# Performance work log

Measured on AMD Instinct MI355X. Metric: run time of the kernel, lower is better.

## Reference

```python
import jax, jax.numpy as jnp
import numpy as np
from jax import lax

B, IMG, ED, NC = 32, 224, 256, 10
DI, DS, DC, DR = 512, 64, 4, 16   # d_inner, d_state, d_conv, dt_rank
NB, L = 6, (IMG // 16) ** 2       # 6 mamba blocks, seq len 196
EPS = 1e-5


def setup_inputs():
    key = jax.random.key(0)
    ks = iter(jax.random.split(key, 48))
    def rn(shape, s=0.02):
        return jax.random.normal(next(ks), shape, jnp.float32) * s
    def ru(shape):
        return jax.random.uniform(next(ks), shape, jnp.float32, 0.5, 1.5)
    inp = {"x": jax.random.normal(next(ks), (B, 3, IMG, IMG), jnp.float32)}
    c = [ED // 4, ED // 2, ED]
    for i, (ci, co) in enumerate([(3, c[0]), (c[0], c[1]), (c[1], c[2])], 1):
        inp[f"c{i}w"] = rn((co, ci, 3, 3), 0.05)
        inp[f"c{i}b"] = rn((co,))
        inp[f"b{i}g"] = jnp.ones((co,), jnp.float32)
        inp[f"b{i}b"] = jnp.zeros((co,), jnp.float32)
        inp[f"b{i}m"] = rn((co,))
        inp[f"b{i}v"] = ru((co,))
    inp["ln_g"] = jnp.ones((NB, ED), jnp.float32)
    inp["ln_b"] = jnp.zeros((NB, ED), jnp.float32)
    inp["w_in"] = rn((NB, 2 * DI, ED))
    inp["cw"] = rn((NB, DI, DC), 0.1)
    inp["cb"] = rn((NB, DI))
    inp["w_x"] = rn((NB, DR + 2 * DS, DI))
    inp["w_dt"] = rn((NB, DI, DR), 0.1)
    inp["b_dt"] = rn((NB, DI), 0.5)
    inp["a_log"] = jnp.tile(jnp.log(jnp.arange(1, DS + 1, dtype=jnp.float32)), (NB, DI, 1))
    inp["d_skip"] = jnp.ones((NB, DI), jnp.float32)
    inp["w_out"] = rn((NB, ED, DI))
    inp["fc_w"] = rn((NC, ED))
    inp["fc_b"] = jnp.zeros((NC,), jnp.float32)
    return inp


def _conv2d(x, w, s, p):
    return lax.conv_general_dilated(x, w, (s, s), [(p, p), (p, p)],
                                    dimension_numbers=("NCHW", "OIHW", "NCHW"))


def _bn(x, g, b, m, v):
    sh = (1, -1, 1, 1)
    return (x - m.reshape(sh)) * (g.reshape(sh) / jnp.sqrt(v.reshape(sh) + EPS)) + b.reshape(sh)


def _maxpool(x, k, s, p):
    return lax.reduce_window(x, -jnp.inf, lax.max, (1, 1, k, k), (1, 1, s, s),
                             [(0, 0), (0, 0), (p, p), (p, p)])


def _mamba_block(x, ln_g, ln_b, w_in, cw, cb, w_x, w_dt, b_dt, a_log, d_skip, w_out):
    res = x
    mu = x.mean(-1, keepdims=True)
    var = ((x - mu) ** 2).mean(-1, keepdims=True)
    h = (x - mu) / jnp.sqrt(var + EPS) * ln_g + ln_b
    xz = jnp.einsum("bld,ed->ble", h, w_in)            # [B,L,2*DI]
    xi, z = xz[..., :DI], xz[..., DI:]
    # causal depthwise conv1d (pad left DC-1) + silu
    xt = lax.conv_general_dilated(xi.transpose(0, 2, 1), cw[:, None, :], (1,),
                                  [(DC - 1, 0)], dimension_numbers=("NCH", "OIH", "NCH"),
                                  feature_group_count=DI) + cb[None, :, None]
    xc = jax.nn.silu(xt).transpose(0, 2, 1)            # [B,L,DI]
    dbl = jnp.einsum("bld,ed->ble", xc, w_x)           # [B,L,DR+2*DS]
    dt = jax.nn.softplus(jnp.einsum("blr,dr->bld", dbl[..., :DR], w_dt) + b_dt)
    Bm = dbl[..., DR:DR + DS]                          # [B,L,DS]
    Cm = dbl[..., DR + DS:]                            # [B,L,DS]
    A = -jnp.exp(a_log)                                # [DI,DS]

    def step(hst, ins):
        dt_t, b_t, c_t, x_t = ins                      # [B,DI],[B,DS],[B,DS],[B,DI]
        dA = jnp.exp(dt_t[..., None] * A)              # [B,DI,DS]
        hst = dA * hst + (dt_t * x_t)[..., None] * b_t[:, None, :]
        return hst, jnp.einsum("bds,bs->bd", hst, c_t)

    h0 = jnp.zeros((x.shape[0], DI, DS), x.dtype)
    _, ys = lax.scan(step, h0, (dt.transpose(1, 0, 2), Bm.transpose(1, 0, 2),
                                Cm.transpose(1, 0, 2), xc.transpose(1, 0, 2)))
    y = ys.transpose(1, 0, 2) + d_skip * xc
    y = y * jax.nn.silu(z)
    return jnp.einsum("bld,ed->ble", y, w_out) + res


def reference(x, c1w, c1b, b1g, b1b, b1m, b1v, c2w, c2b, b2g, b2b, b2m, b2v,
              c3w, c3b, b3g, b3b, b3m, b3v, ln_g, ln_b, w_in, cw, cb, w_x,
              w_dt, b_dt, a_log, d_skip, w_out, fc_w, fc_b):
    h = _maxpool(jax.nn.relu(_bn(_conv2d(x, c1w, 2, 1) + c1b.reshape(1, -1, 1, 1), b1g, b1b, b1m, b1v)), 3, 2, 1)
    h = _maxpool(jax.nn.relu(_bn(_conv2d(h, c2w, 1, 1) + c2b.reshape(1, -1, 1, 1), b2g, b2b, b2m, b2v)), 2, 2, 0)
    h = _maxpool(jax.nn.relu(_bn(_conv2d(h, c3w, 1, 1) + c3b.reshape(1, -1, 1, 1), b3g, b3b, b3m, b3v)), 2, 2, 0)
    h = h.reshape(h.shape[0], ED, -1).transpose(0, 2, 1)   # [B,L,ED]
    for i in range(NB):
        h = _mamba_block(h, ln_g[i], ln_b[i], w_in[i], cw[i], cb[i], w_x[i],
                         w_dt[i], b_dt[i], a_log[i], d_skip[i], w_out[i])
    h = h.mean(axis=1)                                     # adaptive avg pool over L
    return h @ fc_w.T + fc_b
```

## Files before the change

kernel.cpp:

```cpp
#include <hip/hip_runtime.h>

typedef __bf16 bf16x8 __attribute__((ext_vector_type(8)));
typedef float f32x4 __attribute__((ext_vector_type(4)));

#define EPS 1e-5f

__device__ __forceinline__ unsigned short f2bu(float f) {
  union { float f; unsigned u; } x; x.f = f;
  unsigned r = x.u + 0x7fffu + ((x.u >> 16) & 1u);
  return (unsigned short)(r >> 16);
}
__device__ __forceinline__ float bu2f(unsigned short u) {
  union { unsigned u; float f; } x; x.u = ((unsigned)u) << 16;
  return x.f;
}

__device__ __forceinline__ void gld16(const void* g, void* l) {
  __builtin_amdgcn_global_load_lds((const __attribute__((address_space(1))) void*)g,
                                   (__attribute__((address_space(3))) void*)l, 16, 0, 0);
}

__global__ __launch_bounds__(256) void k_f2b(const float* __restrict__ in,
                                             unsigned short* __restrict__ out, int n) {
  int i = blockIdx.x * 256 + threadIdx.x;
  if (i < n) out[i] = f2bu(in[i]);
}

template <int CI>
__global__ __launch_bounds__(256) void k_repack(const float* __restrict__ w,
                                                unsigned short* __restrict__ out, int n) {
  int id = blockIdx.x * 256 + threadIdx.x;
  if (id >= n) return;
  int ci = id % CI;
  int tap = (id / CI) % 9;
  int co = id / (9 * CI);
  out[id] = f2bu(w[(co * CI + ci) * 9 + tap]);
}

__global__ __launch_bounds__(256) void k_wdt_t(const float* __restrict__ in,
                                               float* __restrict__ out) {
  int id = blockIdx.x * 256 + threadIdx.x;
  int d = id & 511;
  int r = (id >> 9) & 15;
  int blk = id >> 13;
  out[id] = in[(blk * 512 + d) * 16 + r];
}

__global__ __launch_bounds__(256) void k_conv1a(
    const float* __restrict__ x, const float* __restrict__ w,
    const float* __restrict__ cb, const float* __restrict__ g,
    const float* __restrict__ bb, const float* __restrict__ bm_,
    const float* __restrict__ bv, unsigned short* __restrict__ out) {
  __shared__ float sw[64 * 27];
  __shared__ float sa[64], sb[64];
  for (int i = threadIdx.x; i < 64 * 27; i += 256) sw[i] = w[i];
  if (threadIdx.x < 64) {
    int c = threadIdx.x;
    float alpha = g[c] * rsqrtf(bv[c] + EPS);
    sa[c] = alpha;
    sb[c] = (cb[c] - bm_[c]) * alpha + bb[c];
  }
  __syncthreads();
  int id = blockIdx.x * 256 + threadIdx.x;
  int c = id & 63;
  int t = id >> 6;
  int ox = t % 112; t /= 112;
  int oy = t % 112;
  int b = t / 112;
  const float* xb = x + (size_t)b * 3 * 224 * 224;
  const float* wc = sw + c * 27;
  float acc = 0.f;
#pragma unroll
  for (int ci = 0; ci < 3; ++ci)
#pragma unroll
    for (int ky = 0; ky < 3; ++ky) {
      int iy = oy * 2 - 1 + ky;
      bool vy = (unsigned)iy < 224u;
#pragma unroll
      for (int kx = 0; kx < 3; ++kx) {
        int ix = ox * 2 - 1 + kx;
        float v = (vy && (unsigned)ix < 224u) ? xb[(ci * 224 + iy) * 224 + ix] : 0.f;
        acc = fmaf(v, wc[ci * 9 + ky * 3 + kx], acc);
      }
    }
  out[id] = f2bu(fmaxf(acc * sa[c] + sb[c], 0.f));
}

__global__ __launch_bounds__(256) void k_pool3(const unsigned short* __restrict__ in,
                                               unsigned short* __restrict__ out) {
  int id = blockIdx.x * 256 + threadIdx.x;
  int c = id & 63;
  int t = id >> 6;
  int px = t % 56; t /= 56;
  int py = t % 56;
  int b = t / 56;
  float m = 0.f;
#pragma unroll
  for (int ky = 0; ky < 3; ++ky) {
    int iy = py * 2 - 1 + ky;
    if ((unsigned)iy >= 112u) continue;
#pragma unroll
    for (int kx = 0; kx < 3; ++kx) {
      int ix = px * 2 - 1 + kx;
      if ((unsigned)ix >= 112u) continue;
      m = fmaxf(m, bu2f(in[(((size_t)(b * 112 + iy) * 112) + ix) * 64 + c]));
    }
  }
  out[id] = f2bu(m);
}

template <int H, int Wd, int CI, int CO>
__global__ __launch_bounds__(256) void k_convgemm(
    const unsigned short* __restrict__ In, const unsigned short* __restrict__ Wt,
    const float* __restrict__ cb, const float* __restrict__ g,
    const float* __restrict__ bb, const float* __restrict__ bm_,
    const float* __restrict__ bv, unsigned short* __restrict__ Out) {
  constexpr int K = 9 * CI;
  constexpr int NTN = CO / 64;
  int bm = blockIdx.x / NTN, bn = blockIdx.x - bm * NTN;
  int lane = threadIdx.x & 63, wid = threadIdx.x >> 6;
  int wr = wid >> 1, wc = wid & 1;
  int r0 = bm * 64 + wr * 32 + (lane & 15);
  int r1 = r0 + 16;
  int c0 = bn * 64 + wc * 32 + (lane & 15);
  int koff = (lane >> 4) << 3;
  int ox0 = r0 % Wd; int t0 = r0 / Wd; int oy0 = t0 % H; int b0 = t0 / H;
  int ox1 = r1 % Wd; int t1 = r1 / Wd; int oy1 = t1 % H; int b1 = t1 / H;
  const unsigned short* pb0 = Wt + (size_t)c0 * K + koff;
  const unsigned short* pb1 = Wt + (size_t)(c0 + 16) * K + koff;
  f32x4 acc[2][2] = {};
  for (int k0 = 0; k0 < K; k0 += 32) {
    int k = k0 + koff;
    int tap = k / CI;
    int ci = k - tap * CI;
    int ky = tap / 3, kx = tap - ky * 3;
    int iy0 = oy0 + ky - 1, ix0 = ox0 + kx - 1;
    int iy1 = oy1 + ky - 1, ix1 = ox1 + kx - 1;
    bf16x8 a0 = {};
    bf16x8 a1 = {};
    if ((unsigned)iy0 < (unsigned)H && (unsigned)ix0 < (unsigned)Wd)
      a0 = *(const bf16x8*)(In + ((size_t)((b0 * H + iy0) * Wd + ix0)) * CI + ci);
    if ((unsigned)iy1 < (unsigned)H && (unsigned)ix1 < (unsigned)Wd)
      a1 = *(const bf16x8*)(In + ((size_t)((b1 * H + iy1) * Wd + ix1)) * CI + ci);
    bf16x8 w0 = *(const bf16x8*)(pb0 + k0);
    bf16x8 w1 = *(const bf16x8*)(pb1 + k0);
    acc[0][0] = __builtin_amdgcn_mfma_f32_16x16x32_bf16(a0, w0, acc[0][0], 0, 0, 0);
    acc[0][1] = __builtin_amdgcn_mfma_f32_16x16x32_bf16(a0, w1, acc[0][1], 0, 0, 0);
    acc[1][0] = __builtin_amdgcn_mfma_f32_16x16x32_bf16(a1, w0, acc[1][0], 0, 0, 0);
    acc[1][1] = __builtin_amdgcn_mfma_f32_16x16x32_bf16(a1, w1, acc[1][1], 0, 0, 0);
  }
  int rr = (lane >> 4) * 4, rc = lane & 15;
#pragma unroll
  for (int tj = 0; tj < 2; ++tj) {
    int col = bn * 64 + wc * 32 + tj * 16 + rc;
    float alpha = g[col] * rsqrtf(bv[col] + EPS);
    float beta = (cb[col] - bm_[col]) * alpha + bb[col];
#pragma unroll
    for (int ti = 0; ti < 2; ++ti) {
      int row = bm * 64 + wr * 32 + ti * 16 + rr;
#pragma unroll
      for (int r = 0; r < 4; ++r) {
        float v = fmaxf(acc[ti][tj][r] * alpha + beta, 0.f);
        Out[(size_t)(row + r) * CO + col] = f2bu(v);
      }
    }
  }
}

template <int H, int Wd, int C, bool OUTF>
__global__ __launch_bounds__(256) void k_pool(const unsigned short* __restrict__ in,
                                              void* __restrict__ outv) {
  constexpr int OH = H / 2, OW = Wd / 2;
  int id = blockIdx.x * 256 + threadIdx.x;
  int c = id % C;
  int t = id / C;
  int px = t % OW; t /= OW;
  int py = t % OH;
  int b = t / OH;
  const unsigned short* p = in + (((size_t)(b * H + py * 2) * Wd) + px * 2) * C + c;
  float m0 = bu2f(p[0]), m1 = bu2f(p[C]);
  float m2 = bu2f(p[(size_t)Wd * C]), m3 = bu2f(p[(size_t)Wd * C + C]);
  float m = fmaxf(fmaxf(m0, m1), fmaxf(m2, m3));
  if (OUTF) ((float*)outv)[id] = m;
  else ((unsigned short*)outv)[id] = f2bu(m);
}

__global__ __launch_bounds__(256) void k_ln(const float* __restrict__ h,
                                            const float* __restrict__ g,
                                            const float* __restrict__ b2,
                                            unsigned short* __restrict__ out) {
  int lane = threadIdx.x & 63, wid = threadIdx.x >> 6;
  int t = blockIdx.x * 4 + wid;
  float4 v = *(const float4*)(h + (size_t)t * 256 + lane * 4);
  float s = v.x + v.y + v.z + v.w;
  float q = v.x * v.x + v.y * v.y + v.z * v.z + v.w * v.w;
#pragma unroll
  for (int off = 32; off; off >>= 1) {
    s += __shfl_xor(s, off);
    q += __shfl_xor(q, off);
  }
  float mu = s * (1.f / 256.f);
  float var = q * (1.f / 256.f) - mu * mu;
  float rs = rsqrtf(var + EPS);
  float4 gg = *(const float4*)(g + lane * 4);
  float4 bb = *(const float4*)(b2 + lane * 4);
  ushort4 o;
  o.x = f2bu((v.x - mu) * rs * gg.x + bb.x);
  o.y = f2bu((v.y - mu) * rs * gg.y + bb.y);
  o.z = f2bu((v.z - mu) * rs * gg.z + bb.z);
  o.w = f2bu((v.w - mu) * rs * gg.w + bb.w);
  *(ushort4*)(out + (size_t)t * 256 + lane * 4) = o;
}

template <int BM, int BN, int KSTEPS, bool ADD>
__global__ __launch_bounds__(256) void k_sgemm(const unsigned short* __restrict__ A,
                                               const unsigned short* __restrict__ W,
                                               float* __restrict__ C,
                                               int N, int ntn) {
  constexpr int K = KSTEPS * 64;
  constexpr int MR = BM / 32;
  constexpr int NR = BN / 32;
  __shared__ __align__(16) unsigned short As[BM * 64];
  __shared__ __align__(16) unsigned short Bs[BN * 64];
  int bm = blockIdx.x / ntn, bn = blockIdx.x - bm * ntn;
  int lane = threadIdx.x & 63, wid = threadIdx.x >> 6;
  int wr = wid >> 1, wc = wid & 1;
  const int arow = lane >> 3, acol = (lane & 7) * 8;
  f32x4 acc[MR][NR] = {};
  const unsigned short* Abase = A + (size_t)(bm * BM) * K;
  const unsigned short* Wbase = W + (size_t)(bn * BN) * K;
  for (int t = 0; t < KSTEPS; ++t) {
    int k0 = t * 64;
#pragma unroll
    for (int i = 0; i < BM / 32; ++i) {
      int chunk = wid * (BM / 32) + i;
      gld16(Abase + (size_t)(chunk * 8 + arow) * K + k0 + acol, &As[chunk * 512 + lane * 8]);
    }
#pragma unroll
    for (int i = 0; i < BN / 32; ++i) {
      int chunk = wid * (BN / 32) + i;
      gld16(Wbase + (size_t)(chunk * 8 + arow) * K + k0 + acol, &Bs[chunk * 512 + lane * 8]);
    }
    __syncthreads();
#pragma unroll
    for (int kk = 0; kk < 2; ++kk) {
      bf16x8 af[MR], bfr[NR];
#pragma unroll
      for (int mi = 0; mi < MR; ++mi)
        af[mi] = *(const bf16x8*)&As[(wr * (BM / 2) + mi * 16 + (lane & 15)) * 64 + kk * 32 + (lane >> 4) * 8];
#pragma unroll
      for (int nj = 0; nj < NR; ++nj)
        bfr[nj] = *(const bf16x8*)&Bs[(wc * (BN / 2) + nj * 16 + (lane & 15)) * 64 + kk * 32 + (lane >> 4) * 8];
#pragma unroll
      for (int mi = 0; mi < MR; ++mi)
#pragma unroll
        for (int nj = 0; nj < NR; ++nj)
          acc[mi][nj] = __builtin_amdgcn_mfma_f32_16x16x32_bf16(af[mi], bfr[nj], acc[mi][nj], 0, 0, 0);
    }
    __syncthreads();
  }
  int rr = (lane >> 4) * 4, rc = lane & 15;
#pragma unroll
  for (int mi = 0; mi < MR; ++mi)
#pragma unroll
    for (int nj = 0; nj < NR; ++nj) {
      int row = bm * BM + wr * (BM / 2) + mi * 16 + rr;
      int col = bn * BN + wc * (BN / 2) + nj * 16 + rc;
#pragma unroll
      for (int r = 0; r < 4; ++r) {
        float v = acc[mi][nj][r];
        if (ADD) v += C[(size_t)(row + r) * N + col];
        C[(size_t)(row + r) * N + col] = v;
      }
    }
}

template <bool ADD_RES>
__global__ __launch_bounds__(256) void k_gemm(const unsigned short* __restrict__ A,
                                              const unsigned short* __restrict__ W,
                                              float* __restrict__ C, int M, int N,
                                              int K, int ntn) {
  int bm = blockIdx.x / ntn, bn = blockIdx.x - bm * ntn;
  int lane = threadIdx.x & 63, wid = threadIdx.x >> 6;
  int wr = wid >> 1, wc = wid & 1;
  int r0 = bm * 64 + wr * 32 + (lane & 15);
  int c0 = bn * 64 + wc * 32 + (lane & 15);
  int koff = (lane >> 4) << 3;
  int cc0 = (c0 < N) ? c0 : (N - 1);
  int cc1 = (c0 + 16 < N) ? (c0 + 16) : (N - 1);
  const unsigned short* pa0 = A + (size_t)r0 * K + koff;
  const unsigned short* pa1 = A + (size_t)(r0 + 16) * K + koff;
  const unsigned short* pb0 = W + (size_t)cc0 * K + koff;
  const unsigned short* pb1 = W + (size_t)cc1 * K + koff;
  f32x4 acc[2][2] = {};
  for (int k0 = 0; k0 < K; k0 += 32) {
    bf16x8 a0 = *(const bf16x8*)(pa0 + k0);
    bf16x8 a1 = *(const bf16x8*)(pa1 + k0);
    bf16x8 b0 = *(const bf16x8*)(pb0 + k0);
    bf16x8 b1 = *(const bf16x8*)(pb1 + k0);
    acc[0][0] = __builtin_amdgcn_mfma_f32_16x16x32_bf16(a0, b0, acc[0][0], 0, 0, 0);
    acc[0][1] = __builtin_amdgcn_mfma_f32_16x16x32_bf16(a0, b1, acc[0][1], 0, 0, 0);
    acc[1][0] = __builtin_amdgcn_mfma_f32_16x16x32_bf16(a1, b0, acc[1][0], 0, 0, 0);
    acc[1][1] = __builtin_amdgcn_mfma_f32_16x16x32_bf16(a1, b1, acc[1][1], 0, 0, 0);
  }
  int rr = (lane >> 4) * 4, rc = lane & 15;
#pragma unroll
  for (int ti = 0; ti < 2; ++ti)
#pragma unroll
    for (int tj = 0; tj < 2; ++tj) {
      int col = bn * 64 + wc * 32 + tj * 16 + rc;
      if (col >= N) continue;
      int row = bm * 64 + wr * 32 + ti * 16 + rr;
#pragma unroll
      for (int r = 0; r < 4; ++r) {
        float v = acc[ti][tj][r];
        if (ADD_RES) v += C[(size_t)(row + r) * N + col];
        C[(size_t)(row + r) * N + col] = v;
      }
    }
}

__global__ __launch_bounds__(256) void k_dwconv(const float* __restrict__ xz,
                                                const float* __restrict__ cw,
                                                const float* __restrict__ cb,
                                                float* __restrict__ xc,
                                                unsigned short* __restrict__ xcb) {
  int id = blockIdx.x * 256 + threadIdx.x;
  int d = id & 511;
  int bl = id >> 9;
  int l = bl % 196;
  int b = bl / 196;
  const float* xi = xz + (size_t)(b * 196) * 1024 + d;
  float4 c4 = *(const float4*)(cw + d * 4);
  float acc = cb[d];
  if (l >= 3) acc = fmaf(xi[(size_t)(l - 3) * 1024], c4.x, acc);
  if (l >= 2) acc = fmaf(xi[(size_t)(l - 2) * 1024], c4.y, acc);
  if (l >= 1) acc = fmaf(xi[(size_t)(l - 1) * 1024], c4.z, acc);
  acc = fmaf(xi[(size_t)l * 1024], c4.w, acc);
  float s = acc / (1.f + __expf(-acc));
  xc[id] = s;
  xcb[id] = f2bu(s);
}

__global__ __launch_bounds__(256) void k_dt(const float* __restrict__ dbl,
                                            const float* __restrict__ wt,
                                            const float* __restrict__ bdt,
                                            float* __restrict__ dt) {
  int id = blockIdx.x * 256 + threadIdx.x;
  int d = id & 511;
  int bl = id >> 9;
  const float4* a = (const float4*)(dbl + (size_t)bl * 144);
  float acc = bdt[d];
#pragma unroll
  for (int i = 0; i < 4; ++i) {
    float4 av = a[i];
    acc = fmaf(av.x, wt[(i * 4 + 0) * 512 + d], acc);
    acc = fmaf(av.y, wt[(i * 4 + 1) * 512 + d], acc);
    acc = fmaf(av.z, wt[(i * 4 + 2) * 512 + d], acc);
    acc = fmaf(av.w, wt[(i * 4 + 3) * 512 + d], acc);
  }
  dt[id] = fmaxf(acc, 0.f) + log1pf(__expf(-fabsf(acc)));
}

__global__ __launch_bounds__(256) void k_scan(
    const float* __restrict__ dtb, const float* __restrict__ xc,
    const float* __restrict__ dbl, const float* __restrict__ xz,
    const float* __restrict__ a_log, const float* __restrict__ d_skip,
    unsigned short* __restrict__ y) {
  __shared__ float lds[4][584];
  int lane = threadIdx.x & 63, wid = threadIdx.x >> 6;
  int wgid = blockIdx.x * 4 + wid;
  int b = wgid >> 9, d = wgid & 511;
  float A = -__expf(a_log[d * 64 + lane]);
  float dsk = d_skip[d];
  const float* dt_p = dtb + (size_t)(b * 196) * 512 + d;
  const float* xc_p = xc + (size_t)(b * 196) * 512 + d;
  const float* z_p = xz + (size_t)(b * 196) * 1024 + 512 + d;
  const float* bc_p = dbl + (size_t)(b * 196) * 144 + 16 + lane;
  unsigned short* y_p = y + (size_t)(b * 196) * 512 + d;
  float* L = lds[wid];
  float h = 0.f;
  int g = lane >> 3, j = lane & 7;
  for (int l0 = 0; l0 < 196; l0 += 8) {
    float p[8];
#pragma unroll
    for (int li = 0; li < 8; ++li) {
      int l = l0 + li;
      bool ok = (l < 196);
      float dtv = ok ? dt_p[(size_t)l * 512] : 0.f;
      float xv = ok ? xc_p[(size_t)l * 512] : 0.f;
      float Bv = ok ? bc_p[(size_t)l * 144] : 0.f;
      float Cv = ok ? bc_p[(size_t)l * 144 + 64] : 0.f;
      float dA = __expf(dtv * A);
      h = fmaf(dA, h, (dtv * xv) * Bv);
      p[li] = h * Cv;
    }
#pragma unroll
    for (int li = 0; li < 8; ++li) L[lane * 9 + li] = p[li];
    __builtin_amdgcn_wave_barrier();
    float s = 0.f;
#pragma unroll
    for (int k = 0; k < 8; ++k) s += L[(j * 8 + k) * 9 + g];
    __builtin_amdgcn_wave_barrier();
    s += __shfl_xor(s, 1);
    s += __shfl_xor(s, 2);
    s += __shfl_xor(s, 4);
    int l = l0 + g;
    if (j == 0 && l < 196) {
      float xv = xc_p[(size_t)l * 512];
      float zv = z_p[(size_t)l * 1024];
      float sig = 1.f / (1.f + __expf(-zv));
      y_p[(size_t)l * 512] = f2bu((s + dsk * xv) * (zv * sig));
    }
  }
}

__global__ __launch_bounds__(256) void k_mean(const float* __restrict__ h,
                                              float* __restrict__ pooled) {
  int b = blockIdx.x, e = threadIdx.x;
  float s = 0.f;
  for (int l = 0; l < 196; ++l) s += h[(size_t)(b * 196 + l) * 256 + e];
  pooled[b * 256 + e] = s * (1.f / 196.f);
}

__global__ __launch_bounds__(320) void k_fc(const float* __restrict__ pooled,
                                            const float* __restrict__ fw,
                                            const float* __restrict__ fb,
                                            float* __restrict__ out) {
  int t = threadIdx.x;
  if (t >= 320) return;
  int b = t / 10, n = t - b * 10;
  float s = fb[n];
  for (int e = 0; e < 256; ++e) s += pooled[b * 256 + e] * fw[n * 256 + e];
  out[t] = s;
}

static inline unsigned cdiv(unsigned a, unsigned b) { return (a + b - 1) / b; }

extern "C" void kernel_launch(void* const* d_in, const int* in_sizes, int n_in,
                              void* d_out, int out_size, void* d_ws, size_t ws_size,
                              hipStream_t stream) {
  const float* x = (const float*)d_in[0];
  const float* c1w = (const float*)d_in[1]; const float* c1b = (const float*)d_in[2];
  const float* b1g = (const float*)d_in[3]; const float* b1b = (const float*)d_in[4];
  const float* b1m = (const float*)d_in[5]; const float* b1v = (const float*)d_in[6];
  const float* c2w = (const float*)d_in[7]; const float* c2b = (const float*)d_in[8];
  const float* b2g = (const float*)d_in[9]; const float* b2b = (const float*)d_in[10];
  const float* b2m = (const float*)d_in[11]; const float* b2v = (const float*)d_in[12];
  const float* c3w = (const float*)d_in[13]; const float* c3b = (const float*)d_in[14];
  const float* b3g = (const float*)d_in[15]; const float* b3b = (const float*)d_in[16];
  const float* b3m = (const float*)d_in[17]; const float* b3v = (const float*)d_in[18];
  const float* ln_g = (const float*)d_in[19]; const float* ln_b = (const float*)d_in[20];
  const float* w_in = (const float*)d_in[21];
  const float* cw = (const float*)d_in[22]; const float* cbv = (const float*)d_in[23];
  const float* w_x = (const float*)d_in[24];
  const float* w_dt = (const float*)d_in[25]; const float* b_dt = (const float*)d_in[26];
  const float* a_log = (const float*)d_in[27]; const float* d_skip = (const float*)d_in[28];
  const float* w_out = (const float*)d_in[29];
  const float* fc_w = (const float*)d_in[30]; const float* fc_b = (const float*)d_in[31];

  char* ws = (char*)d_ws;
  size_t off = 0;
  auto take = [&](size_t bytes) { size_t o = off; off += bytes; return o; };
  size_t S = take(67837952);
  unsigned short* c1o = (unsigned short*)(ws + S + 0);
  unsigned short* t1 = (unsigned short*)(ws + S + 51380224);
  unsigned short* t2 = (unsigned short*)(ws + S + 0);
  unsigned short* t3 = (unsigned short*)(ws + S + 25690112);
  unsigned short* t4 = (unsigned short*)(ws + S + 32112640);
  float* xz = (float*)(ws + S + 0);
  float* xc = (float*)(ws + S + 25690112);
  unsigned short* xcb = (unsigned short*)(ws + S + 38535168);
  float* dbl = (float*)(ws + S + 44957696);
  float* dtb = (float*)(ws + S + 48570368);
  unsigned short* ybf = (unsigned short*)(ws + S + 61415424);
  float* h = (float*)(ws + take(6422528));
  unsigned short* hbf = (unsigned short*)(ws + take(3211264));
  unsigned short* w_in_bf = (unsigned short*)(ws + take(3145728));
  unsigned short* w_x_bf = (unsigned short*)(ws + take(884736));
  unsigned short* w_out_bf = (unsigned short*)(ws + take(1572864));
  unsigned short* w2p = (unsigned short*)(ws + take(147456));
  unsigned short* w3p = (unsigned short*)(ws + take(589824));
  float* wdt_t = (float*)(ws + take(196608));
  float* pooled = (float*)(ws + take(32768));
  (void)ws_size; (void)in_sizes; (void)n_in; (void)out_size;

  k_f2b<<<cdiv(1572864, 256), 256, 0, stream>>>(w_in, w_in_bf, 1572864);
  k_f2b<<<cdiv(442368, 256), 256, 0, stream>>>(w_x, w_x_bf, 442368);
  k_f2b<<<cdiv(786432, 256), 256, 0, stream>>>(w_out, w_out_bf, 786432);
  k_repack<64><<<cdiv(73728, 256), 256, 0, stream>>>(c2w, w2p, 73728);
  k_repack<128><<<cdiv(294912, 256), 256, 0, stream>>>(c3w, w3p, 294912);
  k_wdt_t<<<cdiv(49152, 256), 256, 0, stream>>>(w_dt, wdt_t);

  k_conv1a<<<100352, 256, 0, stream>>>(x, c1w, c1b, b1g, b1b, b1m, b1v, c1o);
  k_pool3<<<25088, 256, 0, stream>>>(c1o, t1);
  k_convgemm<56, 56, 64, 128><<<1568 * 2, 256, 0, stream>>>(t1, w2p, c2b, b2g, b2b, b2m, b2v, t2);
  k_pool<56, 56, 128, false><<<12544, 256, 0, stream>>>(t2, t3);
  k_convgemm<28, 28, 128, 256><<<392 * 4, 256, 0, stream>>>(t3, w3p, c3b, b3g, b3b, b3m, b3v, t4);
  k_pool<28, 28, 256, true><<<6272, 256, 0, stream>>>(t4, h);

  for (int blk = 0; blk < 6; ++blk) {
    k_ln<<<1568, 256, 0, stream>>>(h, ln_g + blk * 256, ln_b + blk * 256, hbf);
    k_sgemm<128, 128, 4, false><<<49 * 8, 256, 0, stream>>>(
        hbf, w_in_bf + (size_t)blk * 1024 * 256, xz, 1024, 8);
    k_dwconv<<<12544, 256, 0, stream>>>(xz, cw + blk * 512 * 4, cbv + blk * 512, xc, xcb);
    k_gemm<false><<<98 * 3, 256, 0, stream>>>(xcb, w_x_bf + (size_t)blk * 144 * 512, dbl,
                                              6272, 144, 512, 3);
    k_dt<<<12544, 256, 0, stream>>>(dbl, wdt_t + blk * 8192, b_dt + blk * 512, dtb);
    k_scan<<<4096, 256, 0, stream>>>(dtb, xc, dbl, xz, a_log + blk * 512 * 64,
                                     d_skip + blk * 512, ybf);
    k_sgemm<64, 64, 8, true><<<98 * 4, 256, 0, stream>>>(
        ybf, w_out_bf + (size_t)blk * 256 * 512, h, 256, 4);
  }

  k_mean<<<32, 256, 0, stream>>>(h, pooled);
  k_fc<<<1, 320, 0, stream>>>(pooled, fc_w, fc_b, (float*)d_out);
}
```

Before: 1.939 ms.

## Merge weight-prep launches, specialize conv1 interior path, parallelize pooling head

Six separate weight conversion and repack kernels are merged into one k_prep launch that dispatches on a flat index. The first conv kernel now copies its weights into registers and takes a branch-free path for interior pixels, keeping the bounds-checked path only for edge pixels. The mean-pool and FC head are split across 128 blocks for partial sums, then finished by a per-batch block that uses wave shuffles, replacing the single-block serial FC. Together these aim to cut launch count and serial tail work, at the cost of a few extra index computations and some duplicated code.

```diff
diff --git a/kernel.cpp b/kernel.cpp
--- a/kernel.cpp
+++ b/kernel.cpp
@@ -20,30 +20,36 @@
                                    (__attribute__((address_space(3))) void*)l, 16, 0, 0);
 }
 
-__global__ __launch_bounds__(256) void k_f2b(const float* __restrict__ in,
-                                             unsigned short* __restrict__ out, int n) {
-  int i = blockIdx.x * 256 + threadIdx.x;
-  if (i < n) out[i] = f2bu(in[i]);
-}
-
-template <int CI>
-__global__ __launch_bounds__(256) void k_repack(const float* __restrict__ w,
-                                                unsigned short* __restrict__ out, int n) {
+__global__ __launch_bounds__(256) void k_prep(
+    const float* __restrict__ w_in, unsigned short* __restrict__ w_in_bf,
+    const float* __restrict__ w_x, unsigned short* __restrict__ w_x_bf,
+    const float* __restrict__ w_out, unsigned short* __restrict__ w_out_bf,
+    const float* __restrict__ c2w, unsigned short* __restrict__ w2p,
+    const float* __restrict__ c3w, unsigned short* __restrict__ w3p,
+    const float* __restrict__ w_dt, float* __restrict__ wdt_t) {
   int id = blockIdx.x * 256 + threadIdx.x;
-  if (id >= n) return;
-  int ci = id % CI;
-  int tap = (id / CI) % 9;
-  int co = id / (9 * CI);
-  out[id] = f2bu(w[(co * CI + ci) * 9 + tap]);
-}
-
-__global__ __launch_bounds__(256) void k_wdt_t(const float* __restrict__ in,
-                                               float* __restrict__ out) {
-  int id = blockIdx.x * 256 + threadIdx.x;
-  int d = id & 511;
-  int r = (id >> 9) & 15;
-  int blk = id >> 13;
-  out[id] = in[(blk * 512 + d) * 16 + r];
+  if (id < 1572864) { w_in_bf[id] = f2bu(w_in[id]); return; }
+  id -= 1572864;
+  if (id < 442368) { w_x_bf[id] = f2bu(w_x[id]); return; }
+  id -= 442368;
+  if (id < 786432) { w_out_bf[id] = f2bu(w_out[id]); return; }
+  id -= 786432;
+  if (id < 73728) {
+    int ci = id % 64, tap = (id / 64) % 9, co = id / 576;
+    w2p[id] = f2bu(c2w[(co * 64 + ci) * 9 + tap]);
+    return;
+  }
+  id -= 73728;
+  if (id < 294912) {
+    int ci = id % 128, tap = (id / 128) % 9, co = id / 1152;
+    w3p[id] = f2bu(c3w[(co * 128 + ci) * 9 + tap]);
+    return;
+  }
+  id -= 294912;
+  {
+    int d = id & 511, r = (id >> 9) & 15, blk = id >> 13;
+    wdt_t[id] = w_dt[(blk * 512 + d) * 16 + r];
+  }
 }
 
 __global__ __launch_bounds__(256) void k_conv1a(
@@ -67,23 +73,37 @@
   int ox = t % 112; t /= 112;
   int oy = t % 112;
   int b = t / 112;
-  const float* xb = x + (size_t)b * 3 * 224 * 224;
-  const float* wc = sw + c * 27;
+  float wr[27];
+#pragma unroll
+  for (int i = 0; i < 27; ++i) wr[i] = sw[c * 27 + i];
+  float alpha = sa[c], beta = sb[c];
+  const float* base = x + (size_t)b * 3 * 224 * 224 + (oy * 2 - 1) * 224 + (ox * 2 - 1);
   float acc = 0.f;
-#pragma unroll
-  for (int ci = 0; ci < 3; ++ci)
-#pragma unroll
-    for (int ky = 0; ky < 3; ++ky) {
-      int iy = oy * 2 - 1 + ky;
-      bool vy = (unsigned)iy < 224u;
-#pragma unroll
-      for (int kx = 0; kx < 3; ++kx) {
-        int ix = ox * 2 - 1 + kx;
-        float v = (vy && (unsigned)ix < 224u) ? xb[(ci * 224 + iy) * 224 + ix] : 0.f;
-        acc = fmaf(v, wc[ci * 9 + ky * 3 + kx], acc);
+  if (oy >= 1 && ox >= 1) {
+#pragma unroll
+    for (int ci = 0; ci < 3; ++ci)
+#pragma unroll
+      for (int ky = 0; ky < 3; ++ky)
+#pragma unroll
+        for (int kx = 0; kx < 3; ++kx)
+          acc = fmaf(base[ci * 224 * 224 + ky * 224 + kx], wr[ci * 9 + ky * 3 + kx], acc);
+  } else {
+#pragma unroll
+    for (int ci = 0; ci < 3; ++ci)
+#pragma unroll
+      for (int ky = 0; ky < 3; ++ky) {
+        int iy = oy * 2 - 1 + ky;
+        bool vy = (unsigned)iy < 224u;
+#pragma unroll
+        for (int kx = 0; kx < 3; ++kx) {
+          int ix = ox * 2 - 1 + kx;
+          float v = (vy && (unsigned)ix < 224u)
+                        ? x[(size_t)b * 3 * 224 * 224 + (ci * 224 + iy) * 224 + ix] : 0.f;
+          acc = fmaf(v, wr[ci * 9 + ky * 3 + kx], acc);
+        }
       }
-    }
-  out[id] = f2bu(fmaxf(acc * sa[c] + sb[c], 0.f));
+  }
+  out[id] = f2bu(fmaxf(acc * alpha + beta, 0.f));
 }
 
 __global__ __launch_bounds__(256) void k_pool3(const unsigned short* __restrict__ in,
@@ -415,24 +435,38 @@
   }
 }
 
-__global__ __launch_bounds__(256) void k_mean(const float* __restrict__ h,
-                                              float* __restrict__ pooled) {
-  int b = blockIdx.x, e = threadIdx.x;
+__global__ __launch_bounds__(256) void k_mean2(const float* __restrict__ h,
+                                               float* __restrict__ part) {
+  int b = blockIdx.x >> 2, q = blockIdx.x & 3;
+  int e = threadIdx.x;
+  const float* hb = h + ((size_t)b * 196 + q * 49) * 256 + e;
   float s = 0.f;
-  for (int l = 0; l < 196; ++l) s += h[(size_t)(b * 196 + l) * 256 + e];
-  pooled[b * 256 + e] = s * (1.f / 196.f);
-}
-
-__global__ __launch_bounds__(320) void k_fc(const float* __restrict__ pooled,
-                                            const float* __restrict__ fw,
-                                            const float* __restrict__ fb,
-                                            float* __restrict__ out) {
-  int t = threadIdx.x;
-  if (t >= 320) return;
-  int b = t / 10, n = t - b * 10;
-  float s = fb[n];
-  for (int e = 0; e < 256; ++e) s += pooled[b * 256 + e] * fw[n * 256 + e];
-  out[t] = s;
+  for (int l = 0; l < 49; ++l) s += hb[(size_t)l * 256];
+  part[((size_t)b * 4 + q) * 256 + e] = s;
+}
+
+__global__ __launch_bounds__(256) void k_head(const float* __restrict__ part,
+                                              const float* __restrict__ fw,
+                                              const float* __restrict__ fb,
+                                              float* __restrict__ out) {
+  __shared__ float sp[256];
+  int b = blockIdx.x;
+  int tid = threadIdx.x, lane = tid & 63, w = tid >> 6;
+  const float* pb = part + (size_t)b * 4 * 256;
+  sp[tid] = (pb[tid] + pb[256 + tid] + pb[512 + tid] + pb[768 + tid]) * (1.f / 196.f);
+  __syncthreads();
+  for (int n = w; n < 10; n += 4) {
+    float s = 0.f;
+#pragma unroll
+    for (int i = 0; i < 4; ++i) {
+      int e = lane * 4 + i;
+      e = e & 255;
+      s += sp[e] * fw[n * 256 + e];
+    }
+    s += __shfl_xor(s, 1); s += __shfl_xor(s, 2); s += __shfl_xor(s, 4);
+    s += __shfl_xor(s, 8); s += __shfl_xor(s, 16); s += __shfl_xor(s, 32);
+    if (lane == 0) out[b * 10 + n] = s + fb[n];
+  }
 }
 
 static inline unsigned cdiv(unsigned a, unsigned b) { return (a + b - 1) / b; }
@@ -482,15 +516,11 @@
   unsigned short* w2p = (unsigned short*)(ws + take(147456));
   unsigned short* w3p = (unsigned short*)(ws + take(589824));
   float* wdt_t = (float*)(ws + take(196608));
-  float* pooled = (float*)(ws + take(32768));
+  float* part = (float*)(ws + take(131072));
   (void)ws_size; (void)in_sizes; (void)n_in; (void)out_size;
 
-  k_f2b<<<cdiv(1572864, 256), 256, 0, stream>>>(w_in, w_in_bf, 1572864);
-  k_f2b<<<cdiv(442368, 256), 256, 0, stream>>>(w_x, w_x_bf, 442368);
-  k_f2b<<<cdiv(786432, 256), 256, 0, stream>>>(w_out, w_out_bf, 786432);
-  k_repack<64><<<cdiv(73728, 256), 256, 0, stream>>>(c2w, w2p, 73728);
-  k_repack<128><<<cdiv(294912, 256), 256, 0, stream>>>(c3w, w3p, 294912);
-  k_wdt_t<<<cdiv(49152, 256), 256, 0, stream>>>(w_dt, wdt_t);
+  k_prep<<<12576, 256, 0, stream>>>(w_in, w_in_bf, w_x, w_x_bf, w_out, w_out_bf,
+                                    c2w, w2p, c3w, w3p, w_dt, wdt_t);
 
   k_conv1a<<<100352, 256, 0, stream>>>(x, c1w, c1b, b1g, b1b, b1m, b1v, c1o);
   k_pool3<<<25088, 256, 0, stream>>>(c1o, t1);
@@ -513,6 +543,6 @@
         ybf, w_out_bf + (size_t)blk * 256 * 512, h, 256, 4);
   }
 
-  k_mean<<<32, 256, 0, stream>>>(h, pooled);
-  k_fc<<<1, 320, 0, stream>>>(pooled, fc_w, fc_b, (float*)d_out);
-}
+  k_mean2<<<128, 256, 0, stream>>>(h, part);
+  k_head<<<32, 256, 0, stream>>>(part, fc_w, fc_b, (float*)d_out);
+}
```

After: 1.937 ms. No clear change (-0.1%).
